# Kernel tuning notes

Hardware: AMD Instinct MI355X
Metric: run time of the kernel (lower is better)

## Reference

```python
import jax, jax.numpy as jnp
import numpy as np

B, S, H = 1, 2048, 2048
NH, NOPE, ROPE, VHD = 16, 128, 64, 128
QHD = NOPE + ROPE            # 192
QLR, KVLR, FF = 1536, 512, 8192
SCALE = QHD ** -0.5          # rope_scaling is None -> mscale = 1
EPS = 1e-6
THETA = 10000.0


def _rms(x, w):
    return x * jax.lax.rsqrt(jnp.mean(x * x, axis=-1, keepdims=True) + EPS) * w


def _rotate_half(x):
    x1, x2 = x[..., : x.shape[-1] // 2], x[..., x.shape[-1] // 2 :]
    return jnp.concatenate((-x2, x1), axis=-1)


def _rope(x, cos, sin, pos):
    # x: (b, h, s, d). First de-interleave pairs: (even dims | odd dims),
    # matching the reshape/transpose in apply_rotary_pos_emb.
    b, h, s, d = x.shape
    x = x.reshape(b, h, s, d // 2, 2).transpose(0, 1, 2, 4, 3).reshape(b, h, s, d)
    c = cos[pos][:, None]   # (b, 1, s, d)
    sn = sin[pos][:, None]
    return x * c + _rotate_half(x) * sn


def setup_inputs() -> dict:
    key = jax.random.key(0)
    ks = jax.random.split(key, 10)
    w = lambda k, shp: jax.random.normal(k, shp, jnp.float32) * 0.02
    hidden_states = jax.random.normal(ks[0], (B, S, H), jnp.float32)
    position_ids = jnp.tile(jnp.arange(S, dtype=jnp.int32)[None], (B, 1))
    inv_freq = 1.0 / (THETA ** (jnp.arange(0, ROPE, 2, dtype=jnp.float32) / ROPE))
    freqs = jnp.arange(S, dtype=jnp.float32)[:, None] * inv_freq[None, :]
    emb = jnp.concatenate([freqs, freqs], axis=-1)  # (S, ROPE)
    return {
        "hidden_states": hidden_states,
        "sin": jnp.sin(emb),
        "cos": jnp.cos(emb),
        "wq_a": w(ks[1], (H, QLR)),
        "q_a_ln": jnp.ones((QLR,), jnp.float32),
        "wq_b": w(ks[2], (QLR, NH * QHD)),
        "wkv_a": w(ks[3], (H, KVLR + ROPE)),
        "kv_a_ln": jnp.ones((KVLR,), jnp.float32),
        "wkv_b": w(ks[4], (KVLR, NH * (NOPE + VHD))),
        "wo": w(ks[5], (NH * VHD, H)),
        "in_ln": jnp.ones((H,), jnp.float32),
        "post_ln": jnp.ones((H,), jnp.float32),
        "w_gate": w(ks[6], (H, FF)),
        "w_up": w(ks[7], (H, FF)),
        "w_down": w(ks[8], (FF, H)),
        "position_ids": position_ids,
    }


def reference(hidden_states, sin, cos, wq_a, q_a_ln, wq_b, wkv_a, kv_a_ln,
              wkv_b, wo, in_ln, post_ln, w_gate, w_up, w_down, position_ids):
    residual = hidden_states
    x = _rms(hidden_states, in_ln)

    # --- MLA: low-rank Q ---
    q = _rms(x @ wq_a, q_a_ln) @ wq_b                       # (B,S,NH*QHD)
    q = q.reshape(B, S, NH, QHD).transpose(0, 2, 1, 3)      # (B,NH,S,QHD)
    q_nope, q_pe = q[..., :NOPE], q[..., NOPE:]

    # --- low-rank KV with shared (MQA) rope key ---
    ckv = x @ wkv_a                                          # (B,S,KVLR+ROPE)
    k_pe = ckv[..., KVLR:].reshape(B, S, 1, ROPE).transpose(0, 2, 1, 3)
    kv = (_rms(ckv[..., :KVLR], kv_a_ln) @ wkv_b)
    kv = kv.reshape(B, S, NH, NOPE + VHD).transpose(0, 2, 1, 3)
    k_nope, v = kv[..., :NOPE], kv[..., NOPE:]

    q_pe = _rope(q_pe, cos, sin, position_ids)
    k_pe = _rope(k_pe, cos, sin, position_ids)

    qs = jnp.concatenate([q_nope, q_pe], axis=-1)            # (B,NH,S,QHD)
    ks = jnp.concatenate([k_nope, jnp.broadcast_to(k_pe, (B, NH, S, ROPE))], axis=-1)

    scores = jnp.einsum("bhqd,bhkd->bhqk", qs, ks) * SCALE
    causal = jnp.tril(jnp.ones((S, S), bool))
    scores = jnp.where(causal, scores, jnp.finfo(scores.dtype).min)
    attn = jax.nn.softmax(scores, axis=-1)
    out = jnp.einsum("bhqk,bhkd->bhqd", attn, v)
    out = out.transpose(0, 2, 1, 3).reshape(B, S, NH * VHD)
    hidden = residual + out @ wo

    # --- dense gated-SiLU MLP ---
    residual = hidden
    y = _rms(hidden, post_ln)
    mlp = (jax.nn.silu(y @ w_gate) * (y @ w_up)) @ w_down
    return residual + mlp
```

## Files before the change

### kernel.cpp

```cpp
#include <hip/hip_runtime.h>
#include <math.h>

#define ATTN_SCALE 0.07216878364870322f

typedef __attribute__((ext_vector_type(8))) short short8;
typedef __attribute__((ext_vector_type(4))) float floatx4;

__device__ __forceinline__ unsigned short f2bf(float f) {
    union { float f; unsigned int u; } v; v.f = f;
    unsigned int r = v.u + 0x7fffu + ((v.u >> 16) & 1u);
    return (unsigned short)(r >> 16);
}
__device__ __forceinline__ float bf2f(unsigned short h) {
    union { unsigned int u; float f; } v; v.u = ((unsigned int)h) << 16;
    return v.f;
}
__device__ __forceinline__ void gld16(const void* g, void* l) {
    __builtin_amdgcn_global_load_lds(
        (const __attribute__((address_space(1))) unsigned int*)g,
        (__attribute__((address_space(3))) unsigned int*)l, 16, 0, 0);
}

__global__ __launch_bounds__(256) void rms_kernel(
    const float* __restrict__ in, int ld_in,
    const float* __restrict__ w,
    unsigned short* __restrict__ out, int ld_out, int N)
{
    const int row = blockIdx.x;
    const int tid = threadIdx.x;
    const float* x = in + (size_t)row * ld_in;
    float ss = 0.f;
    for (int i = tid * 4; i < N; i += 1024) {
        float4 v = *(const float4*)(x + i);
        ss += v.x * v.x + v.y * v.y + v.z * v.z + v.w * v.w;
    }
    #pragma unroll
    for (int off = 32; off > 0; off >>= 1)
        ss += __shfl_down(ss, off);
    __shared__ float red[4];
    const int lane = tid & 63, wid = tid >> 6;
    if (lane == 0) red[wid] = ss;
    __syncthreads();
    const float tot = red[0] + red[1] + red[2] + red[3];
    const float rs = rsqrtf(tot / (float)N + 1e-6f);
    unsigned short* o = out + (size_t)row * ld_out;
    for (int i = tid * 4; i < N; i += 1024) {
        float4 v = *(const float4*)(x + i);
        float4 wv = *(const float4*)(w + i);
        __align__(8) unsigned short ov[4];
        ov[0] = f2bf(v.x * rs * wv.x);
        ov[1] = f2bf(v.y * rs * wv.y);
        ov[2] = f2bf(v.z * rs * wv.z);
        ov[3] = f2bf(v.w * rs * wv.w);
        *(uint2*)&o[i] = *(uint2*)ov;
    }
}

__global__ __launch_bounds__(256) void cast_transpose_kernel(
    const float* __restrict__ W, unsigned short* __restrict__ Wt,
    int K, int N)
{
    __shared__ float tile[64][65];
    const int tid = threadIdx.x;
    const int kb = blockIdx.y * 64;
    const int nb = blockIdx.x * 64;
    const int r  = tid >> 2;
    const int c0 = (tid & 3) * 16;
    if (nb + 64 <= N) {
        #pragma unroll
        for (int j = 0; j < 16; j += 4)
            *(float4*)&tile[r][c0 + j] =
                *(const float4*)&W[(size_t)(kb + r) * N + nb + c0 + j];
    } else {
        for (int j = 0; j < 16; ++j) {
            int n = nb + c0 + j;
            tile[r][c0 + j] = (n < N) ? W[(size_t)(kb + r) * N + n] : 0.f;
        }
    }
    __syncthreads();
    __align__(16) unsigned short ov[16];
    #pragma unroll
    for (int j = 0; j < 16; ++j) ov[j] = f2bf(tile[c0 + j][r]);
    int4* dst = (int4*)&Wt[(size_t)(nb + r) * K + kb + c0];
    dst[0] = ((int4*)ov)[0];
    dst[1] = ((int4*)ov)[1];
}

__global__ __launch_bounds__(256) void gemm_bf16_kernel(
    const unsigned short* __restrict__ A,
    const unsigned short* __restrict__ Bt,
    float* __restrict__ C,
    unsigned short* __restrict__ Cb,
    const float* __restrict__ R,
    int N, int K)
{
    __shared__ __align__(16) unsigned short As[2][4096];
    __shared__ __align__(16) unsigned short Bs[2][4096];
    const int tid = threadIdx.x;
    const int w  = tid >> 6;
    const int l  = tid & 63;
    const int lm = l & 15;
    const int lk = l >> 4;
    const int row0 = blockIdx.y * 128;
    const int col0 = blockIdx.x * 128;
    const int wm = (w >> 1) * 64;
    const int wn = (w & 1) * 64;
    const int nsplit = gridDim.z;
    const int kz = blockIdx.z;
    const int kchunk = K / nsplit;
    const int kbase = kz * kchunk;

    const unsigned short* a0 = A  + (size_t)(row0 + w * 16 + lm) * K + kbase + lk * 8;
    const unsigned short* a1 = a0 + (size_t)64 * K;
    const unsigned short* b0 = Bt + (size_t)(col0 + w * 16 + lm) * K + kbase + lk * 8;
    const unsigned short* b1 = b0 + (size_t)64 * K;
    const int s0 = w * 512 + l * 8;
    const int s1 = (w + 4) * 512 + l * 8;

    floatx4 acc[4][4];
    #pragma unroll
    for (int i = 0; i < 4; ++i)
        #pragma unroll
        for (int j = 0; j < 4; ++j)
            acc[i][j] = (floatx4){0.f, 0.f, 0.f, 0.f};

    gld16(a0, &As[0][s0]);
    gld16(a1, &As[0][s1]);
    gld16(b0, &Bs[0][s0]);
    gld16(b1, &Bs[0][s1]);
    a0 += 32; a1 += 32; b0 += 32; b1 += 32;
    __syncthreads();

    const int niter = kchunk >> 5;
    int cur = 0;
    for (int t = 0; t < niter; ++t) {
        if (t + 1 < niter) {
            gld16(a0, &As[cur ^ 1][s0]);
            gld16(a1, &As[cur ^ 1][s1]);
            gld16(b0, &Bs[cur ^ 1][s0]);
            gld16(b1, &Bs[cur ^ 1][s1]);
            a0 += 32; a1 += 32; b0 += 32; b1 += 32;
        }
        short8 af[4], bg_[4];
        #pragma unroll
        for (int i = 0; i < 4; ++i)
            af[i] = *(const short8*)&As[cur][((w >> 1) * 4 + i) * 512 + l * 8];
        #pragma unroll
        for (int j = 0; j < 4; ++j)
            bg_[j] = *(const short8*)&Bs[cur][((w & 1) * 4 + j) * 512 + l * 8];
        #pragma unroll
        for (int i = 0; i < 4; ++i)
            #pragma unroll
            for (int j = 0; j < 4; ++j)
                acc[i][j] = __builtin_amdgcn_mfma_f32_16x16x32_bf16(
                    af[i], bg_[j], acc[i][j], 0, 0, 0);
        __syncthreads();
        cur ^= 1;
    }

    const int quad = l >> 4;
    const bool ng = (col0 + 128 > N);
    #pragma unroll
    for (int i = 0; i < 4; ++i) {
        #pragma unroll
        for (int r = 0; r < 4; ++r) {
            const int m = row0 + wm + i * 16 + quad * 4 + r;
            #pragma unroll
            for (int j = 0; j < 4; ++j) {
                const int n = col0 + wn + j * 16 + lm;
                if (ng && n >= N) continue;
                const size_t off = (size_t)m * N + n;
                float v = acc[i][j][r];
                if (nsplit > 1) {
                    if (R && kz == 0) v += R[off];
                    unsafeAtomicAdd(&C[off], v);
                } else if (Cb) {
                    Cb[off] = f2bf(v);
                } else {
                    if (R) v += R[off];
                    C[off] = v;
                }
            }
        }
    }
}

__global__ __launch_bounds__(512) void gemm256_kernel(
    const unsigned short* __restrict__ A,
    const unsigned short* __restrict__ Bt,
    float* __restrict__ C,
    unsigned short* __restrict__ Cb,
    const float* __restrict__ R,
    int N, int K)
{
    __shared__ __align__(16) unsigned short As[2][16384];
    __shared__ __align__(16) unsigned short Bs[2][16384];
    const int tid = threadIdx.x;
    const int w   = tid >> 6;
    const int l   = tid & 63;
    const int lm  = l & 15;
    const int quad = l >> 4;
    const int wm2 = w >> 2;
    const int wn4 = w & 3;

    const int gx = gridDim.x;
    const int nwg = gx * gridDim.y;
    int bid = blockIdx.y * gx + blockIdx.x;
    {
        const int q = nwg >> 3, r = nwg & 7;
        const int xcd = bid & 7, off = bid >> 3;
        bid = (xcd < r ? xcd * (q + 1) : r * (q + 1) + (xcd - r) * q) + off;
    }
    const int row0 = (bid / gx) * 256;
    const int col0 = (bid % gx) * 256;

    const int nsplit = gridDim.z;
    const int kz = blockIdx.z;
    const int kchunk = K / nsplit;
    const int kbase = kz * kchunk;

    const int slk = (tid >> 4) & 7;
    const int srg = tid >> 7;
    const unsigned short* sa = A  + (size_t)(row0 + srg * 16 + lm) * K + kbase + slk * 8;
    const unsigned short* sb = Bt + (size_t)(col0 + srg * 16 + lm) * K + kbase + slk * 8;

    floatx4 acc[8][4];
    #pragma unroll
    for (int i = 0; i < 8; ++i)
        #pragma unroll
        for (int j = 0; j < 4; ++j)
            acc[i][j] = (floatx4){0.f, 0.f, 0.f, 0.f};

    const int nt = kchunk >> 6;
    #pragma unroll
    for (int j = 0; j < 4; ++j) {
        gld16(sa + (size_t)j * 64 * K, (char*)As[0] + j * 8192 + tid * 16);
        gld16(sb + (size_t)j * 64 * K, (char*)Bs[0] + j * 8192 + tid * 16);
    }

    for (int t = 0; t < nt; ++t) {
        const int cur = t & 1;
        if (t + 1 < nt) {
            const size_t ko = (size_t)(t + 1) * 64;
            #pragma unroll
            for (int j = 0; j < 4; ++j) {
                gld16(sa + (size_t)j * 64 * K + ko, (char*)As[cur ^ 1] + j * 8192 + tid * 16);
                gld16(sb + (size_t)j * 64 * K + ko, (char*)Bs[cur ^ 1] + j * 8192 + tid * 16);
            }
            asm volatile("s_waitcnt vmcnt(8)" ::: "memory");
        } else {
            asm volatile("s_waitcnt vmcnt(0)" ::: "memory");
        }
        __builtin_amdgcn_sched_barrier(0);
        __builtin_amdgcn_s_barrier();
        __builtin_amdgcn_sched_barrier(0);

        const char* ab = (const char*)As[cur] + wm2 * 16384 + l * 16;
        const char* bb = (const char*)Bs[cur] + wn4 * 8192  + l * 16;
        #pragma unroll
        for (int c = 0; c < 2; ++c) {
            short8 af[8], bf[4];
            #pragma unroll
            for (int i = 0; i < 8; ++i)
                af[i] = *(const short8*)(ab + i * 2048 + c * 1024);
            #pragma unroll
            for (int j = 0; j < 4; ++j)
                bf[j] = *(const short8*)(bb + j * 2048 + c * 1024);
            __builtin_amdgcn_s_setprio(1);
            #pragma unroll
            for (int i = 0; i < 8; ++i)
                #pragma unroll
                for (int j = 0; j < 4; ++j)
                    acc[i][j] = __builtin_amdgcn_mfma_f32_16x16x32_bf16(
                        af[i], bf[j], acc[i][j], 0, 0, 0);
            __builtin_amdgcn_s_setprio(0);
        }
        __builtin_amdgcn_sched_barrier(0);
        __builtin_amdgcn_s_barrier();
        __builtin_amdgcn_sched_barrier(0);
    }

    #pragma unroll
    for (int i = 0; i < 8; ++i) {
        #pragma unroll
        for (int r = 0; r < 4; ++r) {
            const int m = row0 + wm2 * 128 + i * 16 + quad * 4 + r;
            #pragma unroll
            for (int j = 0; j < 4; ++j) {
                const int n = col0 + wn4 * 64 + j * 16 + lm;
                const size_t off = (size_t)m * N + n;
                float v = acc[i][j][r];
                if (nsplit > 1) {
                    if (R && kz == 0) v += R[off];
                    unsafeAtomicAdd(&C[off], v);
                } else if (Cb) {
                    Cb[off] = f2bf(v);
                } else {
                    if (R) v += R[off];
                    C[off] = v;
                }
            }
        }
    }
}

__global__ __launch_bounds__(256) void rope_q_kernel(
    unsigned short* __restrict__ x,
    const float* __restrict__ cosb, const float* __restrict__ sinb,
    const int* __restrict__ pos_ids)
{
    const int gid = blockIdx.x * 256 + threadIdx.x;
    const int i = gid & 31;
    const int grp = gid >> 5;
    const int hh = grp & 15;
    const int row = grp >> 4;
    unsigned short* base = x + (size_t)row * 3072 + hh * 192 + 128;
    const float x0 = bf2f(base[2 * i]);
    const float x1 = bf2f(base[2 * i + 1]);
    const int p = pos_ids[row];
    const float c = cosb[p * 64 + i];
    const float s = sinb[p * 64 + i];
    __syncthreads();
    base[i]      = f2bf(x0 * c - x1 * s);
    base[32 + i] = f2bf(x1 * c + x0 * s);
}

__global__ __launch_bounds__(256) void rope_kpe_kernel(
    const float* __restrict__ ckv, unsigned short* __restrict__ kpe,
    const float* __restrict__ cosb, const float* __restrict__ sinb,
    const int* __restrict__ pos_ids)
{
    const int gid = blockIdx.x * 256 + threadIdx.x;
    const int i = gid & 31;
    const int row = gid >> 5;
    const float x0 = ckv[(size_t)row * 576 + 512 + 2 * i];
    const float x1 = ckv[(size_t)row * 576 + 512 + 2 * i + 1];
    const int p = pos_ids[row];
    const float c = cosb[p * 64 + i];
    const float s = sinb[p * 64 + i];
    kpe[(size_t)row * 64 + i]      = f2bf(x0 * c - x1 * s);
    kpe[(size_t)row * 64 + 32 + i] = f2bf(x1 * c + x0 * s);
}

__global__ __launch_bounds__(256) void vtrans_kernel(
    const unsigned short* __restrict__ kvb, unsigned short* __restrict__ vtg)
{
    __shared__ unsigned short tile[64][72];
    const int tid = threadIdx.x;
    const int s0 = blockIdx.x * 64;
    const int d0 = blockIdx.y * 64;
    const int h  = blockIdx.z;
    const int r  = tid >> 2;
    const int c0 = (tid & 3) * 16;
    *(int4*)&tile[r][c0] =
        *(const int4*)&kvb[(size_t)(s0 + r) * 4096 + h * 256 + 128 + d0 + c0];
    *(int4*)&tile[r][c0 + 8] =
        *(const int4*)&kvb[(size_t)(s0 + r) * 4096 + h * 256 + 128 + d0 + c0 + 8];
    __syncthreads();
    __align__(16) unsigned short ov[16];
    #pragma unroll
    for (int j = 0; j < 16; ++j) ov[j] = tile[c0 + j][r];
    unsigned short* dst = vtg + ((size_t)(h * 128 + d0 + r)) * 2048 + s0 + c0;
    ((int4*)dst)[0] = ((int4*)ov)[0];
    ((int4*)dst)[1] = ((int4*)ov)[1];
}

__global__ __launch_bounds__(512) void attn_mfma_kernel(
    const unsigned short* __restrict__ qb,
    const unsigned short* __restrict__ kvb,
    const unsigned short* __restrict__ kpe,
    const unsigned short* __restrict__ vtg,
    unsigned short* __restrict__ out)
{
    __shared__ __align__(16) unsigned short Kf[128 * 200];
    __shared__ __align__(16) unsigned short Vt[2][128 * 136];
    __shared__ __align__(16) unsigned short Ps[64 * 136];
    __shared__ float pmax_s[8][64];
    __shared__ float psum_s[8][64];
    __shared__ __align__(16) float m_state[64];
    __shared__ __align__(16) float l_state[64];
    __shared__ __align__(16) float alpha_s[64];
    __shared__ __align__(16) float mnew_s[64];

    const int tid  = threadIdx.x;
    const int w    = tid >> 6;
    const int l    = tid & 63;
    const int l15  = l & 15;
    const int quad = l >> 4;
    const int h    = blockIdx.y;
    const int qs   = (w & 3) * 16;
    const int dh   = (w >> 2) * 64;

    for (int pass = 0; pass < 2; ++pass) {
        const int qt = pass ? (31 - (int)blockIdx.x) : (int)blockIdx.x;
        const int q0 = qt * 64;
        const int ntiles = (qt >> 1) + 1;

        short8 qf[4][6];
        #pragma unroll
        for (int nt = 0; nt < 4; ++nt)
            #pragma unroll
            for (int c = 0; c < 6; ++c)
                qf[nt][c] = *(const short8*)&qb[(size_t)(q0 + nt * 16 + l15) * 3072
                                               + h * 192 + c * 32 + quad * 8];

        floatx4 oacc[4];
        #pragma unroll
        for (int nt = 0; nt < 4; ++nt) oacc[nt] = (floatx4){0.f, 0.f, 0.f, 0.f};
        if (tid < 64) { m_state[tid] = -3e38f; l_state[tid] = 0.f; }

        {
            const int k0 = 0;
            for (int s = w; s < 50; s += 8) {
                unsigned ab = s * 1024 + l * 16;
                unsigned row = ab / 400u;
                unsigned g = (ab - row * 400u) >> 4;
                const unsigned short* src;
                if (g < 16u)      src = kvb + (size_t)(k0 + row) * 4096 + h * 256 + g * 8;
                else if (g < 24u) src = kpe + (size_t)(k0 + row) * 64 + (g - 16u) * 8;
                else              src = kpe + (size_t)(k0 + row) * 64;
                gld16(src, (char*)Kf + ab);
            }
            for (int s = w; s < 34; s += 8) {
                unsigned ab = s * 1024 + l * 16;
                unsigned row = ab / 272u;
                unsigned g = (ab - row * 272u) >> 4;
                const unsigned short* src =
                    vtg + (size_t)(h * 128 + row) * 2048 + k0 + (g < 16u ? g * 8 : 0u);
                gld16(src, (char*)Vt[0] + ab);
            }
        }

        for (int kt = 0; kt < ntiles; ++kt) {
            const int k0 = kt * 128;
            const int vb = kt & 1;
            __syncthreads();

            floatx4 st[4];
            #pragma unroll
            for (int nt = 0; nt < 4; ++nt) st[nt] = (floatx4){0.f, 0.f, 0.f, 0.f};
            #pragma unroll
            for (int c = 0; c < 6; ++c) {
                short8 kf = *(const short8*)&Kf[(w * 16 + l15) * 200 + c * 32 + quad * 8];
                #pragma unroll
                for (int nt = 0; nt < 4; ++nt)
                    st[nt] = __builtin_amdgcn_mfma_f32_16x16x32_bf16(kf, qf[nt][c], st[nt], 0, 0, 0);
            }
            #pragma unroll
            for (int nt = 0; nt < 4; ++nt) {
                const int qq = q0 + nt * 16 + l15;
                float vmax = -3e38f;
                #pragma unroll
                for (int r = 0; r < 4; ++r) {
                    const int kpos = k0 + w * 16 + quad * 4 + r;
                    float v = st[nt][r] * ATTN_SCALE;
                    if (kpos > qq) v = -3e38f;
                    st[nt][r] = v;
                    vmax = fmaxf(vmax, v);
                }
                vmax = fmaxf(vmax, __shfl_xor(vmax, 16));
                vmax = fmaxf(vmax, __shfl_xor(vmax, 32));
                if (quad == 0) pmax_s[w][nt * 16 + l15] = vmax;
            }
            __syncthreads();
            if (tid < 64) {
                float mp = m_state[tid];
                float mn = mp;
                #pragma unroll
                for (int ww = 0; ww < 8; ++ww) mn = fmaxf(mn, pmax_s[ww][tid]);
                alpha_s[tid] = __expf(mp - mn);
                mnew_s[tid] = mn;
                m_state[tid] = mn;
            }
            __syncthreads();

            #pragma unroll
            for (int nt = 0; nt < 4; ++nt) {
                const float mn = mnew_s[nt * 16 + l15];
                float vsum = 0.f;
                __align__(8) unsigned short pb[4];
                #pragma unroll
                for (int r = 0; r < 4; ++r) {
                    float p = __expf(st[nt][r] - mn);
                    vsum += p;
                    pb[r] = f2bf(p);
                }
                *(uint2*)&Ps[(nt * 16 + l15) * 136 + w * 16 + quad * 4] = *(uint2*)pb;
                vsum += __shfl_xor(vsum, 16);
                vsum += __shfl_xor(vsum, 32);
                if (quad == 0) psum_s[w][nt * 16 + l15] = vsum;
            }
            {
                float4 al4 = *(const float4*)&alpha_s[qs + quad * 4];
                #pragma unroll
                for (int nt = 0; nt < 4; ++nt) {
                    oacc[nt][0] *= al4.x; oacc[nt][1] *= al4.y;
                    oacc[nt][2] *= al4.z; oacc[nt][3] *= al4.w;
                }
            }
            __syncthreads();
            if (tid < 64) {
                float acc = 0.f;
                #pragma unroll
                for (int ww = 0; ww < 8; ++ww) acc += psum_s[ww][tid];
                l_state[tid] = l_state[tid] * alpha_s[tid] + acc;
            }
            if (kt + 1 < ntiles) {
                const int k1 = k0 + 128;
                for (int s = w; s < 50; s += 8) {
                    unsigned ab = s * 1024 + l * 16;
                    unsigned row = ab / 400u;
                    unsigned g = (ab - row * 400u) >> 4;
                    const unsigned short* src;
                    if (g < 16u)      src = kvb + (size_t)(k1 + row) * 4096 + h * 256 + g * 8;
                    else if (g < 24u) src = kpe + (size_t)(k1 + row) * 64 + (g - 16u) * 8;
                    else              src = kpe + (size_t)(k1 + row) * 64;
                    gld16(src, (char*)Kf + ab);
                }
                for (int s = w; s < 34; s += 8) {
                    unsigned ab = s * 1024 + l * 16;
                    unsigned row = ab / 272u;
                    unsigned g = (ab - row * 272u) >> 4;
                    const unsigned short* src =
                        vtg + (size_t)(h * 128 + row) * 2048 + k1 + (g < 16u ? g * 8 : 0u);
                    gld16(src, (char*)Vt[vb ^ 1] + ab);
                }
            }
            #pragma unroll
            for (int c = 0; c < 4; ++c) {
                short8 pf = *(const short8*)&Ps[(qs + l15) * 136 + c * 32 + quad * 8];
                #pragma unroll
                for (int nt = 0; nt < 4; ++nt) {
                    short8 vf = *(const short8*)&Vt[vb][(dh + nt * 16 + l15) * 136
                                                       + c * 32 + quad * 8];
                    oacc[nt] = __builtin_amdgcn_mfma_f32_16x16x32_bf16(pf, vf, oacc[nt], 0, 0, 0);
                }
            }
        }
        __syncthreads();

        {
            float4 l4 = *(const float4*)&l_state[qs + quad * 4];
            float inv0 = 1.f / l4.x, inv1 = 1.f / l4.y, inv2 = 1.f / l4.z, inv3 = 1.f / l4.w;
            #pragma unroll
            for (int nt = 0; nt < 4; ++nt) {
                const size_t col = h * 128 + dh + nt * 16 + l15;
                out[(size_t)(q0 + qs + quad * 4 + 0) * 2048 + col] = f2bf(oacc[nt][0] * inv0);
                out[(size_t)(q0 + qs + quad * 4 + 1) * 2048 + col] = f2bf(oacc[nt][1] * inv1);
                out[(size_t)(q0 + qs + quad * 4 + 2) * 2048 + col] = f2bf(oacc[nt][2] * inv2);
                out[(size_t)(q0 + qs + quad * 4 + 3) * 2048 + col] = f2bf(oacc[nt][3] * inv3);
            }
        }
        __syncthreads();
    }
}

__global__ __launch_bounds__(256) void silu_mul_kernel(
    unsigned short* __restrict__ g, const unsigned short* __restrict__ u, int n8)
{
    int i = blockIdx.x * 256 + threadIdx.x;
    if (i >= n8) return;
    int4 gv = ((const int4*)g)[i];
    int4 uv = ((const int4*)u)[i];
    const unsigned short* gs = (const unsigned short*)&gv;
    const unsigned short* us = (const unsigned short*)&uv;
    __align__(16) unsigned short ov[8];
    #pragma unroll
    for (int j = 0; j < 8; ++j) {
        float gf = bf2f(gs[j]), uf = bf2f(us[j]);
        ov[j] = f2bf(gf * uf / (1.f + __expf(-gf)));
    }
    ((int4*)g)[i] = *(int4*)ov;
}

extern "C" void kernel_launch(void* const* d_in, const int* in_sizes, int n_in,
                              void* d_out, int out_size, void* d_ws, size_t ws_size,
                              hipStream_t stream)
{
    (void)in_sizes; (void)n_in; (void)out_size; (void)ws_size;
    const float* hidden  = (const float*)d_in[0];
    const float* sinb    = (const float*)d_in[1];
    const float* cosb    = (const float*)d_in[2];
    const float* wq_a    = (const float*)d_in[3];
    const float* q_a_ln  = (const float*)d_in[4];
    const float* wq_b    = (const float*)d_in[5];
    const float* wkv_a   = (const float*)d_in[6];
    const float* kv_a_ln = (const float*)d_in[7];
    const float* wkv_b   = (const float*)d_in[8];
    const float* wo      = (const float*)d_in[9];
    const float* in_ln   = (const float*)d_in[10];
    const float* post_ln = (const float*)d_in[11];
    const float* w_gate  = (const float*)d_in[12];
    const float* w_up    = (const float*)d_in[13];
    const float* w_down  = (const float*)d_in[14];
    const int*   pos     = (const int*)d_in[15];

    char* wsb = (char*)d_ws;
    size_t used = 0;
    auto alloc = [&](size_t bytes) {
        char* p = wsb + used;
        used += (bytes + 255) & ~(size_t)255;
        return p;
    };
    float* q_a   = (float*)alloc((size_t)2048 * 1536 * 4);
    float* ckv   = (float*)alloc((size_t)2048 * 576 * 4);
    float* h2    = (float*)alloc((size_t)2048 * 2048 * 4);
    unsigned short* xnb  = (unsigned short*)alloc((size_t)2048 * 2048 * 2);
    unsigned short* qab  = (unsigned short*)alloc((size_t)2048 * 1536 * 2);
    unsigned short* kvnb = (unsigned short*)alloc((size_t)2048 * 512 * 2);
    unsigned short* qbb  = (unsigned short*)alloc((size_t)2048 * 3072 * 2);
    unsigned short* kvbb = (unsigned short*)alloc((size_t)2048 * 4096 * 2);
    unsigned short* kpe  = (unsigned short*)alloc((size_t)2048 * 64 * 2);
    unsigned short* vtg  = (unsigned short*)alloc((size_t)16 * 128 * 2048 * 2);
    unsigned short* attb = (unsigned short*)alloc((size_t)2048 * 2048 * 2);
    unsigned short* gb   = (unsigned short*)alloc((size_t)2048 * 8192 * 2);
    unsigned short* ub   = (unsigned short*)alloc((size_t)2048 * 8192 * 2);
    unsigned short* wt   = (unsigned short*)alloc((size_t)16777216 * 2);
    float* outp = (float*)d_out;

    hipMemsetAsync(q_a, 0, (size_t)2048 * 1536 * 4, stream);
    hipMemsetAsync(ckv, 0, (size_t)2048 * 576 * 4, stream);
    hipMemsetAsync(h2, 0, (size_t)2048 * 2048 * 4, stream);
    hipMemsetAsync(outp, 0, (size_t)2048 * 2048 * 4, stream);

    rms_kernel<<<2048, 256, 0, stream>>>(hidden, 2048, in_ln, xnb, 2048, 2048);
    cast_transpose_kernel<<<dim3(24, 32), 256, 0, stream>>>(wq_a, wt, 2048, 1536);
    gemm_bf16_kernel<<<dim3(12, 16, 2), 256, 0, stream>>>(xnb, wt, q_a, nullptr, nullptr, 1536, 2048);
    rms_kernel<<<2048, 256, 0, stream>>>(q_a, 1536, q_a_ln, qab, 1536, 1536);
    cast_transpose_kernel<<<dim3(48, 24), 256, 0, stream>>>(wq_b, wt, 1536, 3072);
    gemm_bf16_kernel<<<dim3(24, 16), 256, 0, stream>>>(qab, wt, nullptr, qbb, nullptr, 3072, 1536);
    cast_transpose_kernel<<<dim3(10, 32), 256, 0, stream>>>(wkv_a, wt, 2048, 576);
    gemm_bf16_kernel<<<dim3(5, 16, 4), 256, 0, stream>>>(xnb, wt, ckv, nullptr, nullptr, 576, 2048);
    rms_kernel<<<2048, 256, 0, stream>>>(ckv, 576, kv_a_ln, kvnb, 512, 512);
    cast_transpose_kernel<<<dim3(64, 8), 256, 0, stream>>>(wkv_b, wt, 512, 4096);
    gemm_bf16_kernel<<<dim3(32, 16), 256, 0, stream>>>(kvnb, wt, nullptr, kvbb, nullptr, 4096, 512);
    rope_q_kernel<<<4096, 256, 0, stream>>>(qbb, cosb, sinb, pos);
    rope_kpe_kernel<<<256, 256, 0, stream>>>(ckv, kpe, cosb, sinb, pos);
    vtrans_kernel<<<dim3(32, 2, 16), 256, 0, stream>>>(kvbb, vtg);
    attn_mfma_kernel<<<dim3(16, 16), 512, 0, stream>>>(qbb, kvbb, kpe, vtg, attb);
    cast_transpose_kernel<<<dim3(32, 32), 256, 0, stream>>>(wo, wt, 2048, 2048);
    gemm256_kernel<<<dim3(8, 8, 4), 512, 0, stream>>>(attb, wt, h2, nullptr, hidden, 2048, 2048);
    rms_kernel<<<2048, 256, 0, stream>>>(h2, 2048, post_ln, xnb, 2048, 2048);
    cast_transpose_kernel<<<dim3(128, 32), 256, 0, stream>>>(w_gate, wt, 2048, 8192);
    gemm256_kernel<<<dim3(32, 8, 1), 512, 0, stream>>>(xnb, wt, nullptr, gb, nullptr, 8192, 2048);
    cast_transpose_kernel<<<dim3(128, 32), 256, 0, stream>>>(w_up, wt, 2048, 8192);
    gemm256_kernel<<<dim3(32, 8, 1), 512, 0, stream>>>(xnb, wt, nullptr, ub, nullptr, 8192, 2048);
    silu_mul_kernel<<<8192, 256, 0, stream>>>(gb, ub, 2097152);
    cast_transpose_kernel<<<dim3(32, 128), 256, 0, stream>>>(w_down, wt, 8192, 2048);
    gemm256_kernel<<<dim3(8, 8, 4), 512, 0, stream>>>(gb, wt, outp, nullptr, h2, 2048, 8192);
}
```

Baseline: 1.067 ms.

## Interleave GEMM prefetch with MFMA phases using finer-grained barriers

Restructures the bf16 GEMM main loop into four phases per K-tile. Each phase loads a slice of A fragments from LDS, issues part of the next tile's global-to-LDS prefetch, and runs a subset of the MFMAs, with barriers between phases. The goal is to spread memory traffic across the compute and shorten the per-tile stall on the whole prefetch. In exchange it adds more barriers per tile, a full vmcnt(0) wait at the end of each tile, and a smaller fragment register footprint.

```diff
diff --git a/kernel.cpp b/kernel.cpp
--- a/kernel.cpp
+++ b/kernel.cpp
@@ -237,47 +237,67 @@
         gld16(sa + (size_t)j * 64 * K, (char*)As[0] + j * 8192 + tid * 16);
         gld16(sb + (size_t)j * 64 * K, (char*)Bs[0] + j * 8192 + tid * 16);
     }
+    asm volatile("s_waitcnt vmcnt(0)" ::: "memory");
+    __builtin_amdgcn_sched_barrier(0);
+    __builtin_amdgcn_s_barrier();
+    __builtin_amdgcn_sched_barrier(0);
 
     for (int t = 0; t < nt; ++t) {
-        const int cur = t & 1;
-        if (t + 1 < nt) {
-            const size_t ko = (size_t)(t + 1) * 64;
-            #pragma unroll
-            for (int j = 0; j < 4; ++j) {
-                gld16(sa + (size_t)j * 64 * K + ko, (char*)As[cur ^ 1] + j * 8192 + tid * 16);
-                gld16(sb + (size_t)j * 64 * K + ko, (char*)Bs[cur ^ 1] + j * 8192 + tid * 16);
-            }
-            asm volatile("s_waitcnt vmcnt(8)" ::: "memory");
-        } else {
-            asm volatile("s_waitcnt vmcnt(0)" ::: "memory");
-        }
-        __builtin_amdgcn_sched_barrier(0);
-        __builtin_amdgcn_s_barrier();
-        __builtin_amdgcn_sched_barrier(0);
-
-        const char* ab = (const char*)As[cur] + wm2 * 16384 + l * 16;
-        const char* bb = (const char*)Bs[cur] + wn4 * 8192  + l * 16;
-        #pragma unroll
-        for (int c = 0; c < 2; ++c) {
-            short8 af[8], bf[4];
-            #pragma unroll
-            for (int i = 0; i < 8; ++i)
-                af[i] = *(const short8*)(ab + i * 2048 + c * 1024);
-            #pragma unroll
-            for (int j = 0; j < 4; ++j)
-                bf[j] = *(const short8*)(bb + j * 2048 + c * 1024);
+        const int p = t & 1;
+        const char* ab = (const char*)As[p] + wm2 * 16384 + l * 16;
+        const char* bb = (const char*)Bs[p] + wn4 * 8192  + l * 16;
+        char* dA = (char*)As[p ^ 1] + tid * 16;
+        char* dB = (char*)Bs[p ^ 1] + tid * 16;
+        const size_t ko = (size_t)(t + 1) * 64;
+        const bool pre = (t + 1 < nt);
+        short8 bfr[4][2];
+        short8 afr[2][2];
+
+        #pragma unroll
+        for (int q = 0; q < 4; ++q) {
+            if (q == 0) {
+                #pragma unroll
+                for (int j = 0; j < 4; ++j) {
+                    bfr[j][0] = *(const short8*)(bb + j * 2048);
+                    bfr[j][1] = *(const short8*)(bb + j * 2048 + 1024);
+                }
+            }
+            afr[0][0] = *(const short8*)(ab + (2 * q) * 2048);
+            afr[0][1] = *(const short8*)(ab + (2 * q) * 2048 + 1024);
+            afr[1][0] = *(const short8*)(ab + (2 * q + 1) * 2048);
+            afr[1][1] = *(const short8*)(ab + (2 * q + 1) * 2048 + 1024);
+            if (pre) {
+                if (q == 0) {
+                    gld16(sa + ko, dA);
+                    gld16(sb + ko, dB);
+                    gld16(sa + (size_t)64 * K + ko, dA + 8192);
+                    gld16(sb + (size_t)64 * K + ko, dB + 8192);
+                } else if (q == 1) {
+                    gld16(sa + (size_t)128 * K + ko, dA + 16384);
+                    gld16(sb + (size_t)128 * K + ko, dB + 16384);
+                    gld16(sa + (size_t)192 * K + ko, dA + 24576);
+                    gld16(sb + (size_t)192 * K + ko, dB + 24576);
+                }
+            }
+            __builtin_amdgcn_sched_barrier(0);
+            __builtin_amdgcn_s_barrier();
+            __builtin_amdgcn_sched_barrier(0);
             __builtin_amdgcn_s_setprio(1);
             #pragma unroll
-            for (int i = 0; i < 8; ++i)
-                #pragma unroll
-                for (int j = 0; j < 4; ++j)
-                    acc[i][j] = __builtin_amdgcn_mfma_f32_16x16x32_bf16(
-                        af[i], bf[j], acc[i][j], 0, 0, 0);
+            for (int c = 0; c < 2; ++c)
+                #pragma unroll
+                for (int i2 = 0; i2 < 2; ++i2)
+                    #pragma unroll
+                    for (int j = 0; j < 4; ++j)
+                        acc[2 * q + i2][j] = __builtin_amdgcn_mfma_f32_16x16x32_bf16(
+                            afr[i2][c], bfr[j][c], acc[2 * q + i2][j], 0, 0, 0);
             __builtin_amdgcn_s_setprio(0);
-        }
-        __builtin_amdgcn_sched_barrier(0);
-        __builtin_amdgcn_s_barrier();
-        __builtin_amdgcn_sched_barrier(0);
+            __builtin_amdgcn_sched_barrier(0);
+            if (q == 3)
+                asm volatile("s_waitcnt vmcnt(0)" ::: "memory");
+            __builtin_amdgcn_s_barrier();
+            __builtin_amdgcn_sched_barrier(0);
+        }
     }
 
     #pragma unroll
```

Measured after the change: 1.070 ms. Within noise of the previous version (+0.3%).
